# Kernel tuning notes

Hardware: AMD Instinct MI355X
Metric: run time of the kernel (lower is better)

Reference implementation:

```python
import jax, jax.numpy as jnp
import numpy as np

N_BATCH = 50000
N_FEATURE = 128
DEPTH = 9
N_TREE = 200
N_NODE = 2 ** (DEPTH + 1) - 1  # complete binary tree, 1023 nodes
N_OUTPUT = 8
TREE_LEAF = -1


def setup_inputs() -> dict:
    key = jax.random.key(0)
    kx, kf, kt, kv = jax.random.split(key, 4)
    x = jax.random.normal(kx, (N_BATCH, N_FEATURE), dtype=jnp.float32)

    n_internal = 2 ** DEPTH - 1
    idx = np.arange(N_NODE)
    internal = idx < n_internal
    cl = np.where(internal, 2 * idx + 1, TREE_LEAF).astype(np.int32)
    cr = np.where(internal, 2 * idx + 2, TREE_LEAF).astype(np.int32)
    children_left = jnp.tile(jnp.asarray(cl)[None, :], (N_TREE, 1))
    children_right = jnp.tile(jnp.asarray(cr)[None, :], (N_TREE, 1))

    # random split features at internal nodes, -2 (undefined) at leaves
    feat_rand = jax.random.randint(kf, (N_TREE, N_NODE), 0, N_FEATURE, dtype=jnp.int32)
    feature = jnp.where(jnp.asarray(internal)[None, :], feat_rand, jnp.int32(-2))

    threshold = jax.random.normal(kt, (N_TREE, N_NODE), dtype=jnp.float32)
    value = jax.random.normal(kv, (N_TREE, N_NODE, N_OUTPUT), dtype=jnp.float32)

    return {
        "x": x,
        "feature": feature,
        "threshold": threshold,
        "children_left": children_left,
        "children_right": children_right,
        "value": value,
    }


def reference(x, feature, threshold, children_left, children_right, value):
    n_batch = x.shape[0]
    n_tree = feature.shape[0]
    tidx = jnp.arange(n_tree)[None, :]  # [1, T] broadcasts against node [B, T]

    # pad x with a zero column; leaf nodes (feature < 0) index this column
    xp = jnp.pad(x, ((0, 0), (0, 1)))  # [B, F+1]

    node = jnp.zeros((n_batch, n_tree), dtype=jnp.int32)  # start at root
    for _ in range(DEPTH):
        feat = feature[tidx, node]                       # [B, T]
        feat = jnp.where(feat < 0, N_FEATURE, feat)
        xval = jnp.take_along_axis(xp, feat, axis=1)     # [B, T]
        split = threshold[tidx, node]                    # [B, T]
        lchild = children_left[tidx, node]               # [B, T]
        rchild = children_right[tidx, node]              # [B, T]
        new_node = jnp.where(xval <= split, lchild, rchild)
        # stay put once a leaf marker (-1) is produced
        node = jnp.where(new_node > TREE_LEAF, new_node, node)

    val = value[tidx, node]          # [B, T, n_output]
    out = jnp.mean(val, axis=1)      # activation: mean over trees -> [B, n_output]
    return out
```

## Files before the change

kernel.cpp:

```cpp
#include <hip/hip_runtime.h>

#define N_BATCH   50000
#define N_FEATURE 128
#define DEPTH     9
#define N_TREE    200
#define N_NODE    1023
#define N_OUTPUT  8

#define BPB     64
#define WAVES   8
#define BLOCK   (WAVES * 64)
#define TPR     8
#define ROUNDS  (N_TREE / TPR)

#define FULL_CHUNKS 768
#define NCHUNK      ((N_BATCH + BPB - 1) / BPB)
#define TAIL_CHUNKS (NCHUNK - FULL_CHUNKS)
#define TAIL_SPLIT  ROUNDS
#define TAIL_BLOCKS (TAIL_CHUNKS * TAIL_SPLIT)
#define GRID        (FULL_CHUNKS + TAIL_BLOCKS)

#define TREE_B  2560
#define REC_B   (WAVES * TREE_B)

__device__ __forceinline__ float readlane_f(float v, int lane) {
    return __int_as_float(__builtin_amdgcn_readlane(__float_as_int(v), lane));
}

__global__ __launch_bounds__(BLOCK, 6)
void tree_kernel(const float* __restrict__ x,
                 const int*   __restrict__ feature,
                 const float* __restrict__ threshold,
                 const float* __restrict__ value,
                 float*       __restrict__ out)
{
    __shared__ float xt[N_FEATURE * BPB];
    __shared__ __align__(16) char recbuf[REC_B];

    const int tid = threadIdx.x;
    const int bid = blockIdx.x;
    const int b   = tid & 63;
    const int g   = tid >> 6;
    char* wbuf = recbuf + g * TREE_B;

    int chunk, r0, r1; bool tail;
    if (bid < FULL_CHUNKS) { chunk = bid; r0 = 0; r1 = ROUNDS; tail = false; }
    else {
        const int t2 = bid - FULL_CHUNKS;
        chunk = FULL_CHUNKS + t2 / TAIL_SPLIT;
        r0 = t2 % TAIL_SPLIT; r1 = r0 + 1; tail = true;
    }

    const float* tpre = threshold + (size_t)(r0 * TPR + g) * N_NODE + b;
    const int*   fpre = feature   + (size_t)(r0 * TPR + g) * N_NODE + b;
    const float* vbase = value + (size_t)(r0 * TPR + g) * N_NODE * N_OUTPUT;

    float thr[8]; int fr[8];
    #pragma unroll
    for (int j = 0; j < 8; ++j) { thr[j] = tpre[j * 64]; fr[j] = fpre[j * 64]; }

    {
        const float4* x4 = (const float4*)x;
        float4* R = (float4*)recbuf;
        #pragma unroll
        for (int rr = 0; rr < 2; ++rr) {
            #pragma unroll
            for (int k = 0; k < 2; ++k) {
                const int j  = tid + k * BLOCK;
                const int bl = j >> 5, f4 = j & 31;
                const int gb = chunk * BPB + rr * 32 + bl;
                float4 v = (gb < N_BATCH) ? x4[(size_t)gb * 32 + f4]
                                          : make_float4(0.f, 0.f, 0.f, 0.f);
                R[bl * 32 + (f4 ^ bl)] = v;
            }
            __syncthreads();
            {
                const int b32 = tid & 31, fc = tid >> 5;
                const int bb = rr * 32 + b32;
                #pragma unroll
                for (int c = 0; c < 2; ++c) {
                    const int f4 = fc * 2 + c;
                    float4 v = R[b32 * 32 + (f4 ^ b32)];
                    xt[(f4 * 4 + 0) * BPB + bb] = v.x;
                    xt[(f4 * 4 + 1) * BPB + bb] = v.y;
                    xt[(f4 * 4 + 2) * BPB + bb] = v.z;
                    xt[(f4 * 4 + 3) * BPB + bb] = v.w;
                }
            }
            __syncthreads();
        }
    }

    float acc[N_OUTPUT];
    #pragma unroll
    for (int o = 0; o < N_OUTPUT; ++o) acc[o] = 0.f;
    float4 vp0 = make_float4(0.f, 0.f, 0.f, 0.f);
    float4 vp1 = make_float4(0.f, 0.f, 0.f, 0.f);

    float*         thS = (float*)wbuf;
    unsigned char* fS  = (unsigned char*)(wbuf + 2048);

    for (int r = r0; r < r1; ++r) {
        #pragma unroll
        for (int j = 0; j < 8; ++j) {
            const int dst = (b + j * 64 - 1) & 511;
            thS[dst] = thr[j];
            fS[dst]  = (unsigned char)fr[j];
        }

        const float th0 = readlane_f(thr[0], 0);
        const int   f0  = __builtin_amdgcn_readlane(fr[0], 0);
        const float cx0 = readlane_f(thr[0], 1);
        const float cy0 = readlane_f(thr[0], 2);
        const int   fl0 = __builtin_amdgcn_readlane(fr[0], 1);
        const int   fh0 = __builtin_amdgcn_readlane(fr[0], 2);

        if (r + 1 < r1) {
            const float* tn = tpre + TPR * N_NODE;
            const int*   fn = fpre + TPR * N_NODE;
            #pragma unroll
            for (int j = 0; j < 8; ++j) { thr[j] = tn[j * 64]; fr[j] = fn[j * 64]; }
            tpre = tn; fpre = fn;
        }

        int   m  = 1;
        float th = th0;
        int   fv = f0;
        float2 c = make_float2(cx0, cy0);
        int   fl = fl0, fh = fh0;
        #pragma unroll
        for (int d = 0; d < DEPTH; ++d) {
            const float xv = xt[fv * BPB + b];
            const int s = (xv > th) ? 1 : 0;
            m = 2 * m + s;
            if (d < DEPTH - 1) {
                th = s ? c.y : c.x;
                fv = s ? fh : fl;
            }
            if (d < DEPTH - 2) {
                c = ((float2*)thS)[m - 1];
                const int k2 = ((unsigned short*)fS)[m - 1];
                fl = k2 & 255; fh = k2 >> 8;
            }
        }
        {
            const float4* vp = (const float4*)(vbase + (size_t)(m - 1) * N_OUTPUT);
            const float4 n0 = vp[0], n1 = vp[1];
            acc[0] += vp0.x; acc[1] += vp0.y; acc[2] += vp0.z; acc[3] += vp0.w;
            acc[4] += vp1.x; acc[5] += vp1.y; acc[6] += vp1.z; acc[7] += vp1.w;
            vp0 = n0; vp1 = n1;
        }
        vbase += (size_t)TPR * N_NODE * N_OUTPUT;
    }
    acc[0] += vp0.x; acc[1] += vp0.y; acc[2] += vp0.z; acc[3] += vp0.w;
    acc[4] += vp1.x; acc[5] += vp1.y; acc[6] += vp1.z; acc[7] += vp1.w;

    __syncthreads();
    float* red = (float*)recbuf;
    {
        float* dst = red + (g * 576 + b * 9);
        #pragma unroll
        for (int o = 0; o < N_OUTPUT; ++o) dst[o] = acc[o];
    }
    __syncthreads();
    {
        const int bl = tid >> 3, o = tid & 7;
        const int bg = chunk * BPB + bl;
        float s = 0.f;
        #pragma unroll
        for (int gg = 0; gg < WAVES; ++gg) s += red[gg * 576 + bl * 9 + o];
        s *= (1.0f / N_TREE);
        if (!tail) {
            out[(size_t)chunk * (BPB * N_OUTPUT) + tid] = s;
        } else if (bg < N_BATCH) {
            atomicAdd(out + (size_t)bg * N_OUTPUT + o, s);
        }
    }
}

extern "C" void kernel_launch(void* const* d_in, const int* in_sizes, int n_in,
                              void* d_out, int out_size, void* d_ws, size_t ws_size,
                              hipStream_t stream) {
    const float* x         = (const float*)d_in[0];
    const int*   feature   = (const int*)d_in[1];
    const float* threshold = (const float*)d_in[2];
    const float* value     = (const float*)d_in[5];
    float* out = (float*)d_out;

    const size_t tail_off = (size_t)FULL_CHUNKS * BPB * N_OUTPUT;
    if ((size_t)out_size > tail_off) {
        hipMemsetAsync(out + tail_off, 0, ((size_t)out_size - tail_off) * sizeof(float), stream);
    }

    tree_kernel<<<dim3(GRID), dim3(BLOCK), 0, stream>>>(x, feature, threshold, value, out);
}
```

Before: 135.2 us.

## Speculatively prefetch grandchild features and restructure tree walk with vectorized node tables

The per-tree traversal is rewritten so the first levels' thresholds and features are broadcast from registers and the x values for all candidate children are gathered ahead of each comparison. Deeper levels read 4-wide node quads (grandchildren) from LDS, shortening the dependent LDS-load chain per level at the cost of more loads and registers. Node tables now load as float4/int4 and features are packed into bytes. The tail split changes from per-round blocks to two halves per chunk, full chunks drop to 512, and occupancy bound drops to 4.

```diff
diff --git a/kernel.cpp b/kernel.cpp
--- a/kernel.cpp
+++ b/kernel.cpp
@@ -13,12 +13,12 @@
 #define TPR     8
 #define ROUNDS  (N_TREE / TPR)
 
-#define FULL_CHUNKS 768
+#define FULL_CHUNKS 512
 #define NCHUNK      ((N_BATCH + BPB - 1) / BPB)
 #define TAIL_CHUNKS (NCHUNK - FULL_CHUNKS)
-#define TAIL_SPLIT  ROUNDS
-#define TAIL_BLOCKS (TAIL_CHUNKS * TAIL_SPLIT)
+#define TAIL_BLOCKS (TAIL_CHUNKS * 2)
 #define GRID        (FULL_CHUNKS + TAIL_BLOCKS)
+#define TAIL_SPLIT_R 13
 
 #define TREE_B  2560
 #define REC_B   (WAVES * TREE_B)
@@ -26,8 +26,11 @@
 __device__ __forceinline__ float readlane_f(float v, int lane) {
     return __int_as_float(__builtin_amdgcn_readlane(__float_as_int(v), lane));
 }
-
-__global__ __launch_bounds__(BLOCK, 6)
+__device__ __forceinline__ unsigned pack4(int4 f) {
+    return (f.x & 255) | ((f.y & 255) << 8) | ((f.z & 255) << 16) | ((unsigned)f.w << 24);
+}
+
+__global__ __launch_bounds__(BLOCK, 4)
 void tree_kernel(const float* __restrict__ x,
                  const int*   __restrict__ feature,
                  const float* __restrict__ threshold,
@@ -47,17 +50,23 @@
     if (bid < FULL_CHUNKS) { chunk = bid; r0 = 0; r1 = ROUNDS; tail = false; }
     else {
         const int t2 = bid - FULL_CHUNKS;
-        chunk = FULL_CHUNKS + t2 / TAIL_SPLIT;
-        r0 = t2 % TAIL_SPLIT; r1 = r0 + 1; tail = true;
-    }
-
-    const float* tpre = threshold + (size_t)(r0 * TPR + g) * N_NODE + b;
-    const int*   fpre = feature   + (size_t)(r0 * TPR + g) * N_NODE + b;
+        chunk = FULL_CHUNKS + (t2 >> 1);
+        if (t2 & 1) { r0 = TAIL_SPLIT_R; r1 = ROUNDS; }
+        else        { r0 = 0;            r1 = TAIL_SPLIT_R; }
+        tail = true;
+    }
+
+    const float* trow  = threshold + (size_t)(r0 * TPR + g) * N_NODE;
+    const int*   frow  = feature   + (size_t)(r0 * TPR + g) * N_NODE;
     const float* vbase = value + (size_t)(r0 * TPR + g) * N_NODE * N_OUTPUT;
 
-    float thr[8]; int fr[8];
-    #pragma unroll
-    for (int j = 0; j < 8; ++j) { thr[j] = tpre[j * 64]; fr[j] = fpre[j * 64]; }
+    float4 tA, tB; int4 fA, fB; float4 rtq; int4 rfq;
+    __builtin_memcpy(&tA, trow + 3 + 4 * b,       16);
+    __builtin_memcpy(&tB, trow + 3 + 4 * b + 256, 16);
+    __builtin_memcpy(&fA, frow + 3 + 4 * b,       16);
+    __builtin_memcpy(&fB, frow + 3 + 4 * b + 256, 16);
+    __builtin_memcpy(&rtq, trow, 16);
+    __builtin_memcpy(&rfq, frow, 16);
 
     {
         const float4* x4 = (const float4*)x;
@@ -101,54 +110,106 @@
     unsigned char* fS  = (unsigned char*)(wbuf + 2048);
 
     for (int r = r0; r < r1; ++r) {
-        #pragma unroll
-        for (int j = 0; j < 8; ++j) {
-            const int dst = (b + j * 64 - 1) & 511;
-            thS[dst] = thr[j];
-            fS[dst]  = (unsigned char)fr[j];
-        }
-
-        const float th0 = readlane_f(thr[0], 0);
-        const int   f0  = __builtin_amdgcn_readlane(fr[0], 0);
-        const float cx0 = readlane_f(thr[0], 1);
-        const float cy0 = readlane_f(thr[0], 2);
-        const int   fl0 = __builtin_amdgcn_readlane(fr[0], 1);
-        const int   fh0 = __builtin_amdgcn_readlane(fr[0], 2);
+        const float rt0 = rtq.x, rt1 = rtq.y, rt2 = rtq.z, rt3 = rtq.w;
+        const int   rf0 = rfq.x, rf1 = rfq.y, rf2 = rfq.z, rf3 = rfq.w;
+        const float t4  = readlane_f(tA.y, 0), t5  = readlane_f(tA.z, 0), t6  = readlane_f(tA.w, 0);
+        const float t7  = readlane_f(tA.x, 1), t8  = readlane_f(tA.y, 1),
+                    t9  = readlane_f(tA.z, 1), t10 = readlane_f(tA.w, 1);
+        const float t11 = readlane_f(tA.x, 2), t12 = readlane_f(tA.y, 2),
+                    t13 = readlane_f(tA.z, 2), t14 = readlane_f(tA.w, 2);
+        const int f4  = __builtin_amdgcn_readlane(fA.y, 0), f5  = __builtin_amdgcn_readlane(fA.z, 0),
+                  f6  = __builtin_amdgcn_readlane(fA.w, 0);
+        const int f7  = __builtin_amdgcn_readlane(fA.x, 1), f8  = __builtin_amdgcn_readlane(fA.y, 1),
+                  f9  = __builtin_amdgcn_readlane(fA.z, 1), f10 = __builtin_amdgcn_readlane(fA.w, 1);
+        const int f11 = __builtin_amdgcn_readlane(fA.x, 2), f12 = __builtin_amdgcn_readlane(fA.y, 2),
+                  f13 = __builtin_amdgcn_readlane(fA.z, 2), f14 = __builtin_amdgcn_readlane(fA.w, 2);
+
+        const float xg0 = xt[rf0 * BPB + b];
+        const float xg1 = xt[rf1 * BPB + b], xg2 = xt[rf2 * BPB + b];
+        const float xg3 = xt[rf3 * BPB + b], xg4 = xt[f4 * BPB + b],
+                    xg5 = xt[f5  * BPB + b], xg6 = xt[f6 * BPB + b];
+
+        ((float4*)thS)[b]        = tA;
+        ((float4*)thS)[b + 64]   = tB;
+        ((unsigned*)fS)[b]       = pack4(fA);
+        ((unsigned*)fS)[b + 64]  = pack4(fB);
 
         if (r + 1 < r1) {
-            const float* tn = tpre + TPR * N_NODE;
-            const int*   fn = fpre + TPR * N_NODE;
-            #pragma unroll
-            for (int j = 0; j < 8; ++j) { thr[j] = tn[j * 64]; fr[j] = fn[j * 64]; }
-            tpre = tn; fpre = fn;
-        }
-
-        int   m  = 1;
-        float th = th0;
-        int   fv = f0;
-        float2 c = make_float2(cx0, cy0);
-        int   fl = fl0, fh = fh0;
-        #pragma unroll
-        for (int d = 0; d < DEPTH; ++d) {
-            const float xv = xt[fv * BPB + b];
-            const int s = (xv > th) ? 1 : 0;
-            m = 2 * m + s;
-            if (d < DEPTH - 1) {
-                th = s ? c.y : c.x;
-                fv = s ? fh : fl;
-            }
-            if (d < DEPTH - 2) {
-                c = ((float2*)thS)[m - 1];
-                const int k2 = ((unsigned short*)fS)[m - 1];
-                fl = k2 & 255; fh = k2 >> 8;
-            }
-        }
+            trow += TPR * N_NODE; frow += TPR * N_NODE;
+            __builtin_memcpy(&tA, trow + 3 + 4 * b,       16);
+            __builtin_memcpy(&tB, trow + 3 + 4 * b + 256, 16);
+            __builtin_memcpy(&fA, frow + 3 + 4 * b,       16);
+            __builtin_memcpy(&fB, frow + 3 + 4 * b + 256, 16);
+            __builtin_memcpy(&rtq, trow, 16);
+            __builtin_memcpy(&rfq, frow, 16);
+        }
+
+        const int s0 = xg0 > rt0;
+        const int n1 = 1 + s0;
+        const int fc0 = s0 ? f11 : f7, fc1 = s0 ? f12 : f8,
+                  fc2 = s0 ? f13 : f9, fc3 = s0 ? f14 : f10;
+        const float xh0 = xt[fc0 * BPB + b], xh1 = xt[fc1 * BPB + b],
+                    xh2 = xt[fc2 * BPB + b], xh3 = xt[fc3 * BPB + b];
+        const float xv1 = s0 ? xg2 : xg1; const float tv1 = s0 ? rt2 : rt1;
+        const int s1 = xv1 > tv1; const int n2 = 2 * n1 + 1 + s1;
+        const float4   q4  = ((const float4*)thS)[n2];
+        const unsigned fq4 = ((const unsigned*)fS)[n2];
+        const float xva = s0 ? xg5 : xg3, xvb = s0 ? xg6 : xg4;
+        const float tva = s0 ? t5 : rt3,  tvb = s0 ? t6 : t4;
+        const float xv2 = s1 ? xvb : xva; const float tv2 = s1 ? tvb : tva;
+        const int s2 = xv2 > tv2; const int n3 = 2 * n2 + 1 + s2;
+        const float4   q5  = ((const float4*)thS)[n3];
+        const unsigned fq5 = ((const unsigned*)fS)[n3];
+        const float ta0 = s0 ? t11 : t7, ta1 = s0 ? t12 : t8,
+                    ta2 = s0 ? t13 : t9, ta3 = s0 ? t14 : t10;
+        const float tb0 = s1 ? ta2 : ta0, tb1 = s1 ? ta3 : ta1;
+        const float xc0 = s1 ? xh2 : xh0, xc1 = s1 ? xh3 : xh1;
+        const float tv3 = s2 ? tb1 : tb0; const float xv3 = s2 ? xc1 : xc0;
+        const int s3 = xv3 > tv3; const int n4 = 2 * n3 + 1 + s3;
+        const float4   q6  = ((const float4*)thS)[n4];
+        const unsigned fq6 = ((const unsigned*)fS)[n4];
+        const float xj0 = xt[(fq4 & 255) * BPB + b], xj1 = xt[((fq4 >> 8) & 255) * BPB + b],
+                    xj2 = xt[((fq4 >> 16) & 255) * BPB + b], xj3 = xt[(fq4 >> 24) * BPB + b];
+        const float u0 = s2 ? q4.z : q4.x, u1 = s2 ? q4.w : q4.y;
+        const float w0 = s2 ? xj2 : xj0,   w1 = s2 ? xj3 : xj1;
+        const float tv4 = s3 ? u1 : u0;    const float xv4 = s3 ? w1 : w0;
+        const int s4 = xv4 > tv4; const int n5 = 2 * n4 + 1 + s4;
+        const float4   q7  = ((const float4*)thS)[n5];
+        const unsigned fq7 = ((const unsigned*)fS)[n5];
+        const float xk0 = xt[(fq5 & 255) * BPB + b], xk1 = xt[((fq5 >> 8) & 255) * BPB + b],
+                    xk2 = xt[((fq5 >> 16) & 255) * BPB + b], xk3 = xt[(fq5 >> 24) * BPB + b];
+        const float u2 = s3 ? q5.z : q5.x, u3 = s3 ? q5.w : q5.y;
+        const float w2 = s3 ? xk2 : xk0,   w3 = s3 ? xk3 : xk1;
+        const float tv5 = s4 ? u3 : u2;    const float xv5 = s4 ? w3 : w2;
+        const int s5 = xv5 > tv5; const int n6 = 2 * n5 + 1 + s5;
+        const float4   q8  = ((const float4*)thS)[n6];
+        const unsigned fq8 = ((const unsigned*)fS)[n6];
+        const float xl0 = xt[(fq6 & 255) * BPB + b], xl1 = xt[((fq6 >> 8) & 255) * BPB + b],
+                    xl2 = xt[((fq6 >> 16) & 255) * BPB + b], xl3 = xt[(fq6 >> 24) * BPB + b];
+        const float u4 = s4 ? q6.z : q6.x, u5 = s4 ? q6.w : q6.y;
+        const float w4 = s4 ? xl2 : xl0,   w5 = s4 ? xl3 : xl1;
+        const float tv6 = s5 ? u5 : u4;    const float xv6 = s5 ? w5 : w4;
+        const int s6 = xv6 > tv6; const int n7 = 2 * n6 + 1 + s6;
+        const float xm0 = xt[(fq7 & 255) * BPB + b], xm1 = xt[((fq7 >> 8) & 255) * BPB + b],
+                    xm2 = xt[((fq7 >> 16) & 255) * BPB + b], xm3 = xt[(fq7 >> 24) * BPB + b];
+        const float u6 = s5 ? q7.z : q7.x, u7 = s5 ? q7.w : q7.y;
+        const float w6 = s5 ? xm2 : xm0,   w7 = s5 ? xm3 : xm1;
+        const float tv7 = s6 ? u7 : u6;    const float xv7 = s6 ? w7 : w6;
+        const int s7 = xv7 > tv7; const int n8 = 2 * n7 + 1 + s7;
+        const float xn0 = xt[(fq8 & 255) * BPB + b], xn1 = xt[((fq8 >> 8) & 255) * BPB + b],
+                    xn2 = xt[((fq8 >> 16) & 255) * BPB + b], xn3 = xt[(fq8 >> 24) * BPB + b];
+        const float u8 = s6 ? q8.z : q8.x, u9 = s6 ? q8.w : q8.y;
+        const float w8 = s6 ? xn2 : xn0,   w9 = s6 ? xn3 : xn1;
+        const float tv8 = s7 ? u9 : u8;    const float xv8 = s7 ? w9 : w8;
+        const int s8 = xv8 > tv8;
+        const int leaf = 2 * n8 + 1 + s8;
+
         {
-            const float4* vp = (const float4*)(vbase + (size_t)(m - 1) * N_OUTPUT);
-            const float4 n0 = vp[0], n1 = vp[1];
+            const float4* vp = (const float4*)(vbase + (size_t)leaf * N_OUTPUT);
+            const float4 n0v = vp[0], n1v = vp[1];
             acc[0] += vp0.x; acc[1] += vp0.y; acc[2] += vp0.z; acc[3] += vp0.w;
             acc[4] += vp1.x; acc[5] += vp1.y; acc[6] += vp1.z; acc[7] += vp1.w;
-            vp0 = n0; vp1 = n1;
+            vp0 = n0v; vp1 = n1v;
         }
         vbase += (size_t)TPR * N_NODE * N_OUTPUT;
     }
```

Result: slower. 149.3 us (+10.4%).
